# Kernel tuning notes

Hardware: AMD Instinct MI355X
Metric: run time of the kernel (lower is better)

## Reference

```python
import jax, jax.numpy as jnp
import numpy as np

N_NODES = 100000
N_EDGES = 1600000
IN_F = 256
OUT_F = 64


def setup_inputs() -> dict:
    key = jax.random.key(0)
    k1, k2, k3, k4, k5 = jax.random.split(key, 5)
    features = jax.random.normal(k1, (N_NODES, IN_F), dtype=jnp.float32)
    # xavier_uniform for [in, out] weight
    limit = float(np.sqrt(6.0 / (IN_F + OUT_F)))
    weight = jax.random.uniform(k2, (IN_F, OUT_F), dtype=jnp.float32, minval=-limit, maxval=limit)
    adj_rows = jnp.sort(jax.random.randint(k3, (N_EDGES,), 0, N_NODES, dtype=jnp.int32))
    adj_cols = jax.random.randint(k4, (N_EDGES,), 0, N_NODES, dtype=jnp.int32)
    # positive edge weights (e.g. normalized adjacency values)
    adj_vals = jax.random.uniform(k5, (N_EDGES,), dtype=jnp.float32) * (1.0 / 16.0)
    return {
        "features": features,
        "weight": weight,
        "adj_rows": adj_rows,
        "adj_cols": adj_cols,
        "adj_vals": adj_vals,
        "active": 1,
    }


def _spmm(rows, cols, vals, x, n_nodes):
    # sparse [N,N] @ dense [N,F]: gather neighbor rows, scale, scatter-add
    gathered = vals[:, None] * x[cols]          # [E, F]
    return jax.ops.segment_sum(gathered, rows, num_segments=n_nodes)


def reference(features, weight, adj_rows, adj_cols, adj_vals, active):
    support = features @ weight                 # [N, out]
    if active:
        support = jnp.tanh(support)
    n = features.shape[0]
    output = _spmm(adj_rows, adj_cols, adj_vals, support, n)  # adj @ support
    az = _spmm(adj_rows, adj_cols, adj_vals, output, n)       # adj @ output
    return (output, az)
```

## Files before the change

kernel.cpp:

```cpp
#include <hip/hip_runtime.h>
#include <hip/hip_bf16.h>
#include <math.h>

#define IN_F  256
#define OUT_F 64
#define PD    264

typedef __attribute__((ext_vector_type(8))) short bf16x8;
typedef __attribute__((ext_vector_type(4))) float f32x4;

__device__ inline unsigned short f2b(float x) {
    union { __hip_bfloat16 h; unsigned short u; } cv;
    cv.h = __float2bfloat16(x);
    return cv.u;
}
__device__ inline float b2f_lo(unsigned int u) { return __uint_as_float(u << 16); }
__device__ inline float b2f_hi(unsigned int u) { return __uint_as_float(u & 0xffff0000u); }

__global__ void rowptr_kernel(const int* __restrict__ rows,
                              int* __restrict__ row_ptr,
                              int n_rows, int n_edges) {
    int r = blockIdx.x * blockDim.x + threadIdx.x;
    if (r > n_rows) return;
    if (r == n_rows) { row_ptr[n_rows] = n_edges; return; }
    int lo = 0, hi = n_edges;
    while (lo < hi) {
        int mid = (lo + hi) >> 1;
        if (rows[mid] < r) lo = mid + 1; else hi = mid;
    }
    row_ptr[r] = lo;
}

__global__ __launch_bounds__(256) void gemm_tanh_kernel(
    const float* __restrict__ feat,
    const float* __restrict__ w,
    const int*  __restrict__ active,
    unsigned short* __restrict__ sup_bf,
    int N)
{
    __shared__ unsigned short wt[OUT_F * PD];

    const int t = threadIdx.x;
    #pragma unroll
    for (int r = 0; r < 16; ++r) {
        int f = r * 256 + t;
        float4 v = ((const float4*)w)[f];
        int k = f >> 4;
        int n = (f & 15) << 2;
        wt[(n + 0) * PD + k] = f2b(v.x);
        wt[(n + 1) * PD + k] = f2b(v.y);
        wt[(n + 2) * PD + k] = f2b(v.z);
        wt[(n + 3) * PD + k] = f2b(v.w);
    }
    __syncthreads();

    const int lane = t & 63;
    const int m    = lane & 15;
    const int quad = lane >> 4;
    const int node0 = blockIdx.x * 256 + (t >> 6) * 64;

    f32x4 acc[4][4];
    #pragma unroll
    for (int a = 0; a < 4; ++a)
        #pragma unroll
        for (int b = 0; b < 4; ++b) acc[a][b] = (f32x4)0.0f;

    const float* arow[4];
    #pragma unroll
    for (int mt = 0; mt < 4; ++mt) {
        int nd = node0 + mt * 16 + m;
        if (nd > N - 1) nd = N - 1;
        arow[mt] = feat + (size_t)nd * IN_F;
    }

    for (int kt = 0; kt < 8; ++kt) {
        const int ko = kt * 32 + quad * 8;
        bf16x8 a[4];
        #pragma unroll
        for (int mt = 0; mt < 4; ++mt) {
            f32x4 lo = *(const f32x4*)(arow[mt] + ko);
            f32x4 hi = *(const f32x4*)(arow[mt] + ko + 4);
            bf16x8 av;
            av[0] = (short)f2b(lo[0]); av[1] = (short)f2b(lo[1]);
            av[2] = (short)f2b(lo[2]); av[3] = (short)f2b(lo[3]);
            av[4] = (short)f2b(hi[0]); av[5] = (short)f2b(hi[1]);
            av[6] = (short)f2b(hi[2]); av[7] = (short)f2b(hi[3]);
            a[mt] = av;
        }
        #pragma unroll
        for (int nt = 0; nt < 4; ++nt) {
            bf16x8 b = *(const bf16x8*)(&wt[(nt * 16 + m) * PD + ko]);
            #pragma unroll
            for (int mt = 0; mt < 4; ++mt)
                acc[mt][nt] = __builtin_amdgcn_mfma_f32_16x16x32_bf16(a[mt], b, acc[mt][nt], 0, 0, 0);
        }
    }

    int act = __builtin_amdgcn_readfirstlane(active[0]);
    #pragma unroll
    for (int mt = 0; mt < 4; ++mt) {
        #pragma unroll
        for (int r = 0; r < 4; ++r) {
            int node = node0 + mt * 16 + quad * 4 + r;
            if (node >= N) continue;
            #pragma unroll
            for (int nt = 0; nt < 4; ++nt) {
                float v = acc[mt][nt][r];
                if (act) v = tanhf(v);
                sup_bf[(size_t)node * OUT_F + nt * 16 + m] = f2b(v);
            }
        }
    }
}

__device__ inline int lower_bound(const int* __restrict__ a, int n, int key) {
    int lo = 0, hi = n;
    while (lo < hi) {
        int mid = (lo + hi) >> 1;
        if (a[mid] < key) lo = mid + 1; else hi = mid;
    }
    return lo;
}

template <bool XBF>
__global__ __launch_bounds__(256) void spmm_kernel(
    const int* __restrict__ row_ptr,
    const int* __restrict__ rows,
    const int* __restrict__ cols,
    const float* __restrict__ vals,
    const void* __restrict__ x,
    float* __restrict__ out,
    unsigned short* __restrict__ out_bf,
    int N, int E)
{
    const int wv   = __builtin_amdgcn_readfirstlane((int)(threadIdx.x >> 6));
    const int row  = blockIdx.x * 4 + wv;
    const int lane = threadIdx.x & 63;
    const int h    = lane >> 5;
    const int l    = lane & 31;
    if (row >= N) return;

    int s, e;
    if (row_ptr) { s = row_ptr[row]; e = row_ptr[row + 1]; }
    else         { s = lower_bound(rows, E, row); e = lower_bound(rows, E, row + 1); }

    const unsigned short* xb = (const unsigned short*)x;
    const float*          xf = (const float*)x;

    float ax = 0.0f, ay = 0.0f;
    int i = s;
    for (; i + 8 <= e; i += 8) {
        #pragma unroll
        for (int p = 0; p < 4; ++p) {
            int   c0 = cols[i + 2 * p],     c1 = cols[i + 2 * p + 1];
            float v0 = vals[i + 2 * p],     v1 = vals[i + 2 * p + 1];
            int   c  = h ? c1 : c0;
            float v  = h ? v1 : v0;
            if (XBF) {
                unsigned int r2 = *(const unsigned int*)(xb + (size_t)c * OUT_F + 2 * l);
                ax = fmaf(v, b2f_lo(r2), ax);
                ay = fmaf(v, b2f_hi(r2), ay);
            } else {
                float2 r2 = *(const float2*)(xf + (size_t)c * OUT_F + 2 * l);
                ax = fmaf(v, r2.x, ax);
                ay = fmaf(v, r2.y, ay);
            }
        }
    }
    for (; i + 2 <= e; i += 2) {
        int   c0 = cols[i],  c1 = cols[i + 1];
        float v0 = vals[i],  v1 = vals[i + 1];
        int   c  = h ? c1 : c0;
        float v  = h ? v1 : v0;
        if (XBF) {
            unsigned int r2 = *(const unsigned int*)(xb + (size_t)c * OUT_F + 2 * l);
            ax = fmaf(v, b2f_lo(r2), ax);
            ay = fmaf(v, b2f_hi(r2), ay);
        } else {
            float2 r2 = *(const float2*)(xf + (size_t)c * OUT_F + 2 * l);
            ax = fmaf(v, r2.x, ax);
            ay = fmaf(v, r2.y, ay);
        }
    }
    if (i < e) {
        int   c = cols[i];
        float v = h ? 0.0f : vals[i];
        if (XBF) {
            unsigned int r2 = *(const unsigned int*)(xb + (size_t)c * OUT_F + 2 * l);
            ax = fmaf(v, b2f_lo(r2), ax);
            ay = fmaf(v, b2f_hi(r2), ay);
        } else {
            float2 r2 = *(const float2*)(xf + (size_t)c * OUT_F + 2 * l);
            ax = fmaf(v, r2.x, ax);
            ay = fmaf(v, r2.y, ay);
        }
    }

    ax += __shfl_xor(ax, 32, 64);
    ay += __shfl_xor(ay, 32, 64);

    if (h == 0) {
        size_t base = (size_t)row * OUT_F + 2 * l;
        *(float2*)(out + base) = make_float2(ax, ay);
        if (out_bf) {
            unsigned int pk = (unsigned int)f2b(ax) | ((unsigned int)f2b(ay) << 16);
            *(unsigned int*)(out_bf + base) = pk;
        }
    }
}

extern "C" void kernel_launch(void* const* d_in, const int* in_sizes, int n_in,
                              void* d_out, int out_size, void* d_ws, size_t ws_size,
                              hipStream_t stream) {
    const float* feat   = (const float*)d_in[0];
    const float* w      = (const float*)d_in[1];
    const int*   rows   = (const int*)d_in[2];
    const int*   cols   = (const int*)d_in[3];
    const float* vals   = (const float*)d_in[4];
    const int*   active = (const int*)d_in[5];

    const int N = in_sizes[0] / IN_F;
    const int E = in_sizes[2];

    float* out = (float*)d_out;
    float* az  = out + (size_t)N * OUT_F;

    size_t rp_bytes = (((size_t)(N + 1) * sizeof(int)) + 255) & ~(size_t)255;
    size_t bf_bytes = (((size_t)N * OUT_F * sizeof(unsigned short)) + 255) & ~(size_t)255;
    char* ws = (char*)d_ws;

    int* row_ptr = (ws_size >= rp_bytes) ? (int*)ws : nullptr;
    size_t used = row_ptr ? rp_bytes : 0;

    unsigned short* sup_bf;
    unsigned short* mid_bf = nullptr;
    if (ws_size >= used + 2 * bf_bytes) {
        sup_bf = (unsigned short*)(ws + used);
        mid_bf = (unsigned short*)(ws + used + bf_bytes);
    } else if (ws_size >= used + bf_bytes) {
        sup_bf = (unsigned short*)(ws + used);
    } else {
        sup_bf = (unsigned short*)az;
    }

    if (row_ptr) {
        int threads = N + 1;
        rowptr_kernel<<<(threads + 255) / 256, 256, 0, stream>>>(rows, row_ptr, N, E);
    }

    {
        int blocks = (N + 255) / 256;
        gemm_tanh_kernel<<<blocks, 256, 0, stream>>>(feat, w, active, sup_bf, N);
    }

    int spmm_blocks = (N + 3) / 4;
    spmm_kernel<true><<<spmm_blocks, 256, 0, stream>>>(
        row_ptr, rows, cols, vals, sup_bf, out, mid_bf, N, E);
    if (mid_bf) {
        spmm_kernel<true><<<spmm_blocks, 256, 0, stream>>>(
            row_ptr, rows, cols, vals, mid_bf, az, nullptr, N, E);
    } else {
        spmm_kernel<false><<<spmm_blocks, 256, 0, stream>>>(
            row_ptr, rows, cols, vals, out, az, nullptr, N, E);
    }
}
```

Before: 296.7 us.

## Fuse row-pointer build into GEMM launch and widen SpMM gathers to 16-byte loads

Row-pointer construction moves out of its own launch. It now runs as extra blocks of the GEMM kernel and uses an edge-parallel boundary scan instead of a per-row binary search. The GEMM is re-tiled to 512-thread blocks with one 16-row tile per wave, trading the 4x register reuse of A tiles for more parallelism. The SpMM now has each lane gather 8 features with 16-byte loads and handle 8 edges per wave step, reduced by cross-lane shuffles, with nontemporal output stores. This cuts the number of load instructions but adds shuffle reductions and wastes lanes on short rows.

Result: faster. 270.5 us (-8.8%).

```diff
diff --git a/kernel.cpp b/kernel.cpp
--- a/kernel.cpp
+++ b/kernel.cpp
@@ -17,33 +17,34 @@
 __device__ inline float b2f_lo(unsigned int u) { return __uint_as_float(u << 16); }
 __device__ inline float b2f_hi(unsigned int u) { return __uint_as_float(u & 0xffff0000u); }
 
-__global__ void rowptr_kernel(const int* __restrict__ rows,
-                              int* __restrict__ row_ptr,
-                              int n_rows, int n_edges) {
-    int r = blockIdx.x * blockDim.x + threadIdx.x;
-    if (r > n_rows) return;
-    if (r == n_rows) { row_ptr[n_rows] = n_edges; return; }
-    int lo = 0, hi = n_edges;
-    while (lo < hi) {
-        int mid = (lo + hi) >> 1;
-        if (rows[mid] < r) lo = mid + 1; else hi = mid;
-    }
-    row_ptr[r] = lo;
-}
-
-__global__ __launch_bounds__(256) void gemm_tanh_kernel(
+__global__ __launch_bounds__(512) void gemm_rowptr_kernel(
     const float* __restrict__ feat,
     const float* __restrict__ w,
     const int*  __restrict__ active,
+    const int*  __restrict__ rows,
     unsigned short* __restrict__ sup_bf,
-    int N)
+    int* __restrict__ row_ptr,
+    int N, int E, int GB)
 {
     __shared__ unsigned short wt[OUT_F * PD];
 
+    if ((int)blockIdx.x >= GB) {
+        int e = ((int)blockIdx.x - GB) * 512 + (int)threadIdx.x;
+        if (e < E) {
+            int r  = rows[e];
+            int rn = (e + 1 < E) ? rows[e + 1] : N;
+            if (e == 0) {
+                for (int j = 0; j <= r; ++j) row_ptr[j] = 0;
+            }
+            for (int j = r + 1; j <= rn; ++j) row_ptr[j] = e + 1;
+        }
+        return;
+    }
+
     const int t = threadIdx.x;
     #pragma unroll
-    for (int r = 0; r < 16; ++r) {
-        int f = r * 256 + t;
+    for (int r = 0; r < 8; ++r) {
+        int f = r * 512 + t;
         float4 v = ((const float4*)w)[f];
         int k = f >> 4;
         int n = (f & 15) << 2;
@@ -57,58 +58,43 @@
     const int lane = t & 63;
     const int m    = lane & 15;
     const int quad = lane >> 4;
-    const int node0 = blockIdx.x * 256 + (t >> 6) * 64;
-
-    f32x4 acc[4][4];
-    #pragma unroll
-    for (int a = 0; a < 4; ++a)
-        #pragma unroll
-        for (int b = 0; b < 4; ++b) acc[a][b] = (f32x4)0.0f;
-
-    const float* arow[4];
-    #pragma unroll
-    for (int mt = 0; mt < 4; ++mt) {
-        int nd = node0 + mt * 16 + m;
-        if (nd > N - 1) nd = N - 1;
-        arow[mt] = feat + (size_t)nd * IN_F;
-    }
-
+    const int node0 = (int)blockIdx.x * 128 + (t >> 6) * 16;
+
+    int nd = node0 + m;
+    if (nd > N - 1) nd = N - 1;
+    const float* arow = feat + (size_t)nd * IN_F;
+
+    f32x4 acc[4];
+    #pragma unroll
+    for (int b = 0; b < 4; ++b) acc[b] = (f32x4)0.0f;
+
+    #pragma unroll
     for (int kt = 0; kt < 8; ++kt) {
         const int ko = kt * 32 + quad * 8;
-        bf16x8 a[4];
-        #pragma unroll
-        for (int mt = 0; mt < 4; ++mt) {
-            f32x4 lo = *(const f32x4*)(arow[mt] + ko);
-            f32x4 hi = *(const f32x4*)(arow[mt] + ko + 4);
-            bf16x8 av;
-            av[0] = (short)f2b(lo[0]); av[1] = (short)f2b(lo[1]);
-            av[2] = (short)f2b(lo[2]); av[3] = (short)f2b(lo[3]);
-            av[4] = (short)f2b(hi[0]); av[5] = (short)f2b(hi[1]);
-            av[6] = (short)f2b(hi[2]); av[7] = (short)f2b(hi[3]);
-            a[mt] = av;
-        }
+        f32x4 lo = *(const f32x4*)(arow + ko);
+        f32x4 hi = *(const f32x4*)(arow + ko + 4);
+        bf16x8 a;
+        a[0] = (short)f2b(lo[0]); a[1] = (short)f2b(lo[1]);
+        a[2] = (short)f2b(lo[2]); a[3] = (short)f2b(lo[3]);
+        a[4] = (short)f2b(hi[0]); a[5] = (short)f2b(hi[1]);
+        a[6] = (short)f2b(hi[2]); a[7] = (short)f2b(hi[3]);
         #pragma unroll
         for (int nt = 0; nt < 4; ++nt) {
             bf16x8 b = *(const bf16x8*)(&wt[(nt * 16 + m) * PD + ko]);
-            #pragma unroll
-            for (int mt = 0; mt < 4; ++mt)
-                acc[mt][nt] = __builtin_amdgcn_mfma_f32_16x16x32_bf16(a[mt], b, acc[mt][nt], 0, 0, 0);
+            acc[nt] = __builtin_amdgcn_mfma_f32_16x16x32_bf16(a, b, acc[nt], 0, 0, 0);
         }
     }
 
     int act = __builtin_amdgcn_readfirstlane(active[0]);
     #pragma unroll
-    for (int mt = 0; mt < 4; ++mt) {
+    for (int r = 0; r < 4; ++r) {
+        int node = node0 + quad * 4 + r;
+        if (node >= N) continue;
         #pragma unroll
-        for (int r = 0; r < 4; ++r) {
-            int node = node0 + mt * 16 + quad * 4 + r;
-            if (node >= N) continue;
-            #pragma unroll
-            for (int nt = 0; nt < 4; ++nt) {
-                float v = acc[mt][nt][r];
-                if (act) v = tanhf(v);
-                sup_bf[(size_t)node * OUT_F + nt * 16 + m] = f2b(v);
-            }
+        for (int nt = 0; nt < 4; ++nt) {
+            float v = acc[nt][r];
+            if (act) v = tanhf(v);
+            sup_bf[(size_t)node * OUT_F + nt * 16 + m] = f2b(v);
         }
     }
 }
@@ -120,6 +106,19 @@
         if (a[mid] < key) lo = mid + 1; else hi = mid;
     }
     return lo;
+}
+
+__device__ __forceinline__ void fma8b(float v, uint4 g, float* acc) {
+    acc[0] = fmaf(v, b2f_lo(g.x), acc[0]); acc[1] = fmaf(v, b2f_hi(g.x), acc[1]);
+    acc[2] = fmaf(v, b2f_lo(g.y), acc[2]); acc[3] = fmaf(v, b2f_hi(g.y), acc[3]);
+    acc[4] = fmaf(v, b2f_lo(g.z), acc[4]); acc[5] = fmaf(v, b2f_hi(g.z), acc[5]);
+    acc[6] = fmaf(v, b2f_lo(g.w), acc[6]); acc[7] = fmaf(v, b2f_hi(g.w), acc[7]);
+}
+__device__ __forceinline__ void fma8f(float v, float4 lo, float4 hi, float* acc) {
+    acc[0] = fmaf(v, lo.x, acc[0]); acc[1] = fmaf(v, lo.y, acc[1]);
+    acc[2] = fmaf(v, lo.z, acc[2]); acc[3] = fmaf(v, lo.w, acc[3]);
+    acc[4] = fmaf(v, hi.x, acc[4]); acc[5] = fmaf(v, hi.y, acc[5]);
+    acc[6] = fmaf(v, hi.z, acc[6]); acc[7] = fmaf(v, hi.w, acc[7]);
 }
 
 template <bool XBF>
@@ -133,11 +132,10 @@
     unsigned short* __restrict__ out_bf,
     int N, int E)
 {
-    const int wv   = __builtin_amdgcn_readfirstlane((int)(threadIdx.x >> 6));
-    const int row  = blockIdx.x * 4 + wv;
+    const int row  = blockIdx.x * 4 + (threadIdx.x >> 6);
     const int lane = threadIdx.x & 63;
-    const int h    = lane >> 5;
-    const int l    = lane & 31;
+    const int part = lane & 7;
+    const int esl  = lane >> 3;
     if (row >= N) return;
 
     int s, e;
@@ -147,64 +145,72 @@
     const unsigned short* xb = (const unsigned short*)x;
     const float*          xf = (const float*)x;
 
-    float ax = 0.0f, ay = 0.0f;
+    float acc[8] = {0.f, 0.f, 0.f, 0.f, 0.f, 0.f, 0.f, 0.f};
+
     int i = s;
-    for (; i + 8 <= e; i += 8) {
-        #pragma unroll
-        for (int p = 0; p < 4; ++p) {
-            int   c0 = cols[i + 2 * p],     c1 = cols[i + 2 * p + 1];
-            float v0 = vals[i + 2 * p],     v1 = vals[i + 2 * p + 1];
-            int   c  = h ? c1 : c0;
-            float v  = h ? v1 : v0;
-            if (XBF) {
-                unsigned int r2 = *(const unsigned int*)(xb + (size_t)c * OUT_F + 2 * l);
-                ax = fmaf(v, b2f_lo(r2), ax);
-                ay = fmaf(v, b2f_hi(r2), ay);
-            } else {
-                float2 r2 = *(const float2*)(xf + (size_t)c * OUT_F + 2 * l);
-                ax = fmaf(v, r2.x, ax);
-                ay = fmaf(v, r2.y, ay);
-            }
-        }
-    }
-    for (; i + 2 <= e; i += 2) {
-        int   c0 = cols[i],  c1 = cols[i + 1];
-        float v0 = vals[i],  v1 = vals[i + 1];
-        int   c  = h ? c1 : c0;
-        float v  = h ? v1 : v0;
+    for (; i + 16 <= e; i += 16) {
+        int   ea = i + esl,  eb = i + 8 + esl;
+        int   ca = cols[ea], cb = cols[eb];
+        float va = vals[ea], vb = vals[eb];
         if (XBF) {
-            unsigned int r2 = *(const unsigned int*)(xb + (size_t)c * OUT_F + 2 * l);
-            ax = fmaf(v, b2f_lo(r2), ax);
-            ay = fmaf(v, b2f_hi(r2), ay);
+            uint4 ga = *(const uint4*)(xb + (size_t)ca * OUT_F + part * 8);
+            uint4 gb = *(const uint4*)(xb + (size_t)cb * OUT_F + part * 8);
+            fma8b(va, ga, acc);
+            fma8b(vb, gb, acc);
         } else {
-            float2 r2 = *(const float2*)(xf + (size_t)c * OUT_F + 2 * l);
-            ax = fmaf(v, r2.x, ax);
-            ay = fmaf(v, r2.y, ay);
+            const float* pa = xf + (size_t)ca * OUT_F + part * 8;
+            const float* pb = xf + (size_t)cb * OUT_F + part * 8;
+            float4 la = *(const float4*)pa, ha = *(const float4*)(pa + 4);
+            float4 lb = *(const float4*)pb, hb = *(const float4*)(pb + 4);
+            fma8f(va, la, ha, acc);
+            fma8f(vb, lb, hb, acc);
         }
     }
     if (i < e) {
-        int   c = cols[i];
-        float v = h ? 0.0f : vals[i];
+        int   ea = i + esl, eb = i + 8 + esl;
+        float va = 0.f, vb = 0.f;
         if (XBF) {
-            unsigned int r2 = *(const unsigned int*)(xb + (size_t)c * OUT_F + 2 * l);
-            ax = fmaf(v, b2f_lo(r2), ax);
-            ay = fmaf(v, b2f_hi(r2), ay);
+            uint4 ga = make_uint4(0u, 0u, 0u, 0u);
+            uint4 gb = make_uint4(0u, 0u, 0u, 0u);
+            if (ea < e) { int c = cols[ea]; va = vals[ea];
+                          ga = *(const uint4*)(xb + (size_t)c * OUT_F + part * 8); }
+            if (eb < e) { int c = cols[eb]; vb = vals[eb];
+                          gb = *(const uint4*)(xb + (size_t)c * OUT_F + part * 8); }
+            fma8b(va, ga, acc);
+            fma8b(vb, gb, acc);
         } else {
-            float2 r2 = *(const float2*)(xf + (size_t)c * OUT_F + 2 * l);
-            ax = fmaf(v, r2.x, ax);
-            ay = fmaf(v, r2.y, ay);
-        }
-    }
-
-    ax += __shfl_xor(ax, 32, 64);
-    ay += __shfl_xor(ay, 32, 64);
-
-    if (h == 0) {
-        size_t base = (size_t)row * OUT_F + 2 * l;
-        *(float2*)(out + base) = make_float2(ax, ay);
+            float4 la = make_float4(0.f,0.f,0.f,0.f), ha = la, lb = la, hb = la;
+            if (ea < e) { int c = cols[ea]; va = vals[ea];
+                          const float* p = xf + (size_t)c * OUT_F + part * 8;
+                          la = *(const float4*)p; ha = *(const float4*)(p + 4); }
+            if (eb < e) { int c = cols[eb]; vb = vals[eb];
+                          const float* p = xf + (size_t)c * OUT_F + part * 8;
+                          lb = *(const float4*)p; hb = *(const float4*)(p + 4); }
+            fma8f(va, la, ha, acc);
+            fma8f(vb, lb, hb, acc);
+        }
+    }
+
+    #pragma unroll
+    for (int j = 0; j < 8; ++j) {
+        acc[j] += __shfl_xor(acc[j], 8, 64);
+        acc[j] += __shfl_xor(acc[j], 16, 64);
+        acc[j] += __shfl_xor(acc[j], 32, 64);
+    }
+
+    if (esl == 0) {
+        size_t base = (size_t)row * OUT_F + part * 8;
+        f32x4 o0 = {acc[0], acc[1], acc[2], acc[3]};
+        f32x4 o1 = {acc[4], acc[5], acc[6], acc[7]};
+        __builtin_nontemporal_store(o0, (f32x4*)(out + base));
+        __builtin_nontemporal_store(o1, (f32x4*)(out + base + 4));
         if (out_bf) {
-            unsigned int pk = (unsigned int)f2b(ax) | ((unsigned int)f2b(ay) << 16);
-            *(unsigned int*)(out_bf + base) = pk;
+            uint4 pk;
+            pk.x = (unsigned)f2b(acc[0]) | ((unsigned)f2b(acc[1]) << 16);
+            pk.y = (unsigned)f2b(acc[2]) | ((unsigned)f2b(acc[3]) << 16);
+            pk.z = (unsigned)f2b(acc[4]) | ((unsigned)f2b(acc[5]) << 16);
+            pk.w = (unsigned)f2b(acc[6]) | ((unsigned)f2b(acc[7]) << 16);
+            *(uint4*)(out_bf + base) = pk;
         }
     }
 }
@@ -243,14 +249,11 @@
         sup_bf = (unsigned short*)az;
     }
 
-    if (row_ptr) {
-        int threads = N + 1;
-        rowptr_kernel<<<(threads + 255) / 256, 256, 0, stream>>>(rows, row_ptr, N, E);
-    }
-
     {
-        int blocks = (N + 255) / 256;
-        gemm_tanh_kernel<<<blocks, 256, 0, stream>>>(feat, w, active, sup_bf, N);
+        int GB = (N + 127) / 128;
+        int RB = row_ptr ? (E + 511) / 512 : 0;
+        gemm_rowptr_kernel<<<GB + RB, 512, 0, stream>>>(
+            feat, w, active, rows, sup_bf, row_ptr, N, E, GB);
     }
 
     int spmm_blocks = (N + 3) / 4;
```
